# Kernel optimization log

Measured on AMD Instinct MI355X. Metric: run time of the kernel, lower is better.

Reference implementation:

```python
import jax, jax.numpy as jnp
import numpy as np

VOCAB, EMBED, HIDDEN, NCLASS = 50000, 256, 256, 5
B, T = 64, 512


def _lstm_cell(x, h, c, W, U, b):
    # Keras LSTMCell: gate order i, f, g(candidate), o
    z = x @ W + h @ U + b  # [B, 4H]
    i, f, g, o = jnp.split(z, 4, axis=-1)
    i = jax.nn.sigmoid(i)
    f = jax.nn.sigmoid(f)
    g = jnp.tanh(g)
    o = jax.nn.sigmoid(o)
    c_new = f * c + i * g
    h_new = o * jnp.tanh(c_new)
    return h_new, c_new


def _run_stacked(xs, W1, U1, b1, W2, U2, b2):
    # xs: [T, B, E] -> outputs of layer 2: [T, B, H]
    Bb = xs.shape[1]
    H = U1.shape[0]
    zero = jnp.zeros((Bb, H), dtype=xs.dtype)
    init = (zero, zero, zero, zero)

    def step(carry, x_t):
        h1, c1, h2, c2 = carry
        h1, c1 = _lstm_cell(x_t, h1, c1, W1, U1, b1)
        h2, c2 = _lstm_cell(h1, h2, c2, W2, U2, b2)
        return (h1, c1, h2, c2), h2

    _, ys = jax.lax.scan(step, init, xs)
    return ys


def setup_inputs() -> dict:
    key = jax.random.key(0)
    ks = jax.random.split(key, 16)
    s = 0.05

    def mk(k, shape):
        return (jax.random.normal(k, shape, dtype=jnp.float32) * s)

    inp = {
        "tokens": jax.random.randint(ks[0], (B, T), 0, VOCAB, dtype=jnp.int64),
        "embed_table": mk(ks[1], (VOCAB, EMBED)),
        # forward direction, layer 1 and 2
        "fw_W1": mk(ks[2], (EMBED, 4 * HIDDEN)),
        "fw_U1": mk(ks[3], (HIDDEN, 4 * HIDDEN)),
        "fw_b1": jnp.zeros((4 * HIDDEN,), jnp.float32),
        "fw_W2": mk(ks[4], (HIDDEN, 4 * HIDDEN)),
        "fw_U2": mk(ks[5], (HIDDEN, 4 * HIDDEN)),
        "fw_b2": jnp.zeros((4 * HIDDEN,), jnp.float32),
        # backward direction, layer 1 and 2
        "bw_W1": mk(ks[6], (EMBED, 4 * HIDDEN)),
        "bw_U1": mk(ks[7], (HIDDEN, 4 * HIDDEN)),
        "bw_b1": jnp.zeros((4 * HIDDEN,), jnp.float32),
        "bw_W2": mk(ks[8], (HIDDEN, 4 * HIDDEN)),
        "bw_U2": mk(ks[9], (HIDDEN, 4 * HIDDEN)),
        "bw_b2": jnp.zeros((4 * HIDDEN,), jnp.float32),
        # output dense (2H -> 5), softmax
        "dense_W": mk(ks[10], (2 * HIDDEN, NCLASS)),
        "dense_b": jnp.zeros((NCLASS,), jnp.float32),
    }
    return inp


def reference(tokens, embed_table,
              fw_W1, fw_U1, fw_b1, fw_W2, fw_U2, fw_b2,
              bw_W1, bw_U1, bw_b1, bw_W2, bw_U2, bw_b2,
              dense_W, dense_b):
    emb = embed_table[tokens]                    # [B, T, E]
    xs = jnp.swapaxes(emb, 0, 1)                 # [T, B, E]

    ys_fw = _run_stacked(xs, fw_W1, fw_U1, fw_b1, fw_W2, fw_U2, fw_b2)          # [T,B,H]
    ys_bw = _run_stacked(xs[::-1], bw_W1, bw_U1, bw_b1, bw_W2, bw_U2, bw_b2)[::-1]

    feat = jnp.concatenate([ys_fw, ys_bw], axis=-1)   # [T, B, 2H]
    feat = jnp.swapaxes(feat, 0, 1)                   # [B, T, 2H]
    logits = feat @ dense_W + dense_b                 # [B, T, 5]
    return jax.nn.softmax(logits, axis=-1)
```

## Files before the change

### kernel.cpp

```cpp
#include <hip/hip_runtime.h>

typedef __bf16 bf16;
typedef __bf16 bf16x8 __attribute__((ext_vector_type(8)));
typedef float f32x4 __attribute__((ext_vector_type(4)));
typedef unsigned long long u64;

#define T_LEN 512
#define BATCH 64
#define HID 256
#define LDA 520
#define ZLD 68

#define CTRL_BYTES 4096
#define LOG_OFF CTRL_BYTES
#define LOG_BYTES (T_LEN * BATCH * 16 * 5 * 4)
#define RING_OFF (LOG_OFF + LOG_BYTES)
#define HSLOT_U64 4096
#define RING_SLOTS 16
#define RING_U64 (RING_SLOTS * HSLOT_U64)
#define RING_BYTES (4 * RING_U64 * 8)

#define SMEM_A 66560
#define SMEM_Z 17408
#define SMEM_C 4096
#define SMEM_TAIL 576
#define SMEM_BYTES (SMEM_A + SMEM_Z + SMEM_C + SMEM_TAIL)

__device__ inline uint4 cvt8(const float4* s) {
    float4 a = s[0], b = s[1];
    union { uint4 u; bf16 h[8]; } r;
    r.h[0] = (bf16)a.x; r.h[1] = (bf16)a.y; r.h[2] = (bf16)a.z; r.h[3] = (bf16)a.w;
    r.h[4] = (bf16)b.x; r.h[5] = (bf16)b.y; r.h[6] = (bf16)b.z; r.h[7] = (bf16)b.w;
    return r.u;
}

__device__ __forceinline__ void load16(const u64* src, int tid, u64* dst) {
#pragma unroll
    for (int k = 0; k < 16; ++k)
        dst[k] = __hip_atomic_load(src + k * 256 + tid, __ATOMIC_RELAXED, __HIP_MEMORY_SCOPE_AGENT);
}

__device__ __forceinline__ void resolve16(const u64* src, int tid, unsigned ep,
                                          unsigned mask, u64* dst) {
    for (;;) {
        bool ok = true;
#pragma unroll
        for (int k = 0; k < 16; ++k)
            if ((mask >> k) & 1u) ok &= ((((unsigned)dst[k]) & 1u) == ep);
        if (__all(ok)) break;
        load16(src, tid, dst);
    }
}

__global__ void __launch_bounds__(256, 1)
lstm_kernel(const int* __restrict__ tokens,
            const float* __restrict__ embed,
            const float* __restrict__ W1f, const float* __restrict__ U1f, const float* __restrict__ b1f,
            const float* __restrict__ W2f, const float* __restrict__ U2f, const float* __restrict__ b2f,
            const float* __restrict__ W1b, const float* __restrict__ U1b, const float* __restrict__ b1b,
            const float* __restrict__ W2b, const float* __restrict__ U2b, const float* __restrict__ b2b,
            const float* __restrict__ dW,
            char* __restrict__ ws)
{
    extern __shared__ char smem[];
    bf16*  Abuf  = (bf16*)smem;
    float* zLds  = (float*)(smem + SMEM_A);
    float* cLds  = (float*)(smem + SMEM_A + SMEM_Z);
    float* bLds  = (float*)(smem + SMEM_A + SMEM_Z + SMEM_C);
    float* dwLds = bLds + 64;

    const int tid = threadIdx.x;
    const int wg  = blockIdx.x;
    const int dir = wg & 1, layer = (wg >> 1) & 1, sub = wg >> 2;

    const float *Wp, *Up, *bp;
    if (dir == 0) { if (layer == 0) { Wp=W1f; Up=U1f; bp=b1f; } else { Wp=W2f; Up=U2f; bp=b2f; } }
    else          { if (layer == 0) { Wp=W1b; Up=U1b; bp=b1b; } else { Wp=W2b; Up=U2b; bp=b2b; } }

    {
        for (int it = 0; it < 32; ++it) {
            int idx = it * 256 + tid;
            int k = idx >> 4, q4 = idx & 15;
            int g = q4 >> 2, u0 = (q4 & 3) * 4;
            const float* src = (k < 256) ? (Wp + (size_t)k * 1024 + g * 256 + sub * 16 + u0)
                                         : (Up + (size_t)(k - 256) * 1024 + g * 256 + sub * 16 + u0);
            float4 v = *(const float4*)src;
            int c0 = g * 16 + u0;
            Abuf[(c0 + 0) * LDA + k] = (bf16)v.x;
            Abuf[(c0 + 1) * LDA + k] = (bf16)v.y;
            Abuf[(c0 + 2) * LDA + k] = (bf16)v.z;
            Abuf[(c0 + 3) * LDA + k] = (bf16)v.w;
        }
        if (tid < 64) {
            int g = tid >> 4, u = tid & 15;
            bLds[tid] = bp[g * 256 + sub * 16 + u];
        }
        if (tid < 80) {
            int u = tid / 5, c = tid % 5;
            dwLds[tid] = dW[(size_t)(dir * 256 + sub * 16 + u) * 5 + c];
        }
        for (int i = tid; i < 1024; i += 256) cLds[i] = 0.f;
    }
    __syncthreads();

    const int wave = tid >> 6, lane = tid & 63, quad = lane >> 4, ln = lane & 15;
    const int mrow0 = (wave >> 1) * 32, ncol0 = (wave & 1) * 32;
    bf16x8 bfrag[2][16];
#pragma unroll
    for (int nt = 0; nt < 2; ++nt)
#pragma unroll
        for (int kt = 0; kt < 16; ++kt)
            bfrag[nt][kt] = *(const bf16x8*)&Abuf[(ncol0 + nt * 16 + ln) * LDA + kt * 32 + quad * 8];
    __syncthreads();

    u64* ringL1  = (u64*)(ws + RING_OFF) + (size_t)(dir * 2 + 0) * RING_U64;
    u64* ringL2  = (u64*)(ws + RING_OFF) + (size_t)(dir * 2 + 1) * RING_U64;
    u64* ringOwn = (layer == 0) ? ringL1 : ringL2;
    float* logits  = (float*)(ws + LOG_OFF);
    unsigned* prog = (unsigned*)ws + dir * 32;

    const int bA = tid >> 2, qA = tid & 3;
    const unsigned ownMask = 0xFFFFu ^ (1u << sub);
    unsigned progCache = 0u;
    u64 pkPrevW = 0ull;

    float4 pf[16];
    int tokB = 0;
    if (layer == 0) {
        const int tt0 = dir ? (T_LEN - 1) : 0;
        int tokA = tokens[bA * T_LEN + tt0];
        const float4* src = (const float4*)(embed + (size_t)tokA * HID + qA * 64);
#pragma unroll
        for (int j = 0; j < 16; ++j) pf[j] = src[j];
        const int tt1 = dir ? (T_LEN - 2) : 1;
        tokB = tokens[bA * T_LEN + tt1];
    }

    for (int s = 0; s < T_LEN; ++s) {
        u64 hreg[16], xreg[16];
        const u64* ownSrc = ringOwn + (size_t)(s & 15) * HSLOT_U64;
        const u64* xSrc   = ringL1 + (size_t)((s + 1) & 15) * HSLOT_U64;
        if (s > 0) load16(ownSrc, tid, hreg);
        if (layer == 1) load16(xSrc, tid, xreg);

        if (layer == 0 && tid == 0 && s >= 13) {
            unsigned need = (unsigned)(s - 12);
            while (progCache < need)
                progCache = __hip_atomic_load(prog, __ATOMIC_RELAXED, __HIP_MEMORY_SCOPE_AGENT);
        }

        if (s > 0) {
            resolve16(ownSrc, tid, (unsigned)(((s - 1) >> 4) & 1), ownMask, hreg);
        } else {
#pragma unroll
            for (int k = 0; k < 16; ++k) hreg[k] = 0ull;
        }
        hreg[sub] = pkPrevW;

        if (layer == 0) {
            uint4* dstx = (uint4*)&Abuf[bA * LDA + qA * 64];
#pragma unroll
            for (int j = 0; j < 8; ++j) dstx[j] = cvt8(&pf[2 * j]);
        } else {
            resolve16(xSrc, tid, (unsigned)((s >> 4) & 1), 0xFFFFu, xreg);
#pragma unroll
            for (int k = 0; k < 16; ++k)
                *(u64*)&Abuf[bA * LDA + k * 16 + qA * 4] = xreg[k];
        }
#pragma unroll
        for (int k = 0; k < 16; ++k)
            *(u64*)&Abuf[bA * LDA + 256 + k * 16 + qA * 4] = hreg[k];
        __syncthreads();

        if (layer == 0) {
            const float4* src = (const float4*)(embed + (size_t)tokB * HID + qA * 64);
#pragma unroll
            for (int j = 0; j < 16; ++j) pf[j] = src[j];
            const int sn2 = (s + 2 < T_LEN) ? s + 2 : T_LEN - 1;
            const int tt2 = dir ? (T_LEN - 1 - sn2) : sn2;
            tokB = tokens[bA * T_LEN + tt2];
        }

        f32x4 acc[2][2];
#pragma unroll
        for (int mi = 0; mi < 2; ++mi)
#pragma unroll
            for (int ni = 0; ni < 2; ++ni) acc[mi][ni] = (f32x4)(0.0f);
#pragma unroll
        for (int kt = 0; kt < 16; ++kt) {
            bf16x8 a0 = *(const bf16x8*)&Abuf[(mrow0 + ln) * LDA + kt * 32 + quad * 8];
            bf16x8 a1 = *(const bf16x8*)&Abuf[(mrow0 + 16 + ln) * LDA + kt * 32 + quad * 8];
            acc[0][0] = __builtin_amdgcn_mfma_f32_16x16x32_bf16(a0, bfrag[0][kt], acc[0][0], 0, 0, 0);
            acc[0][1] = __builtin_amdgcn_mfma_f32_16x16x32_bf16(a0, bfrag[1][kt], acc[0][1], 0, 0, 0);
            acc[1][0] = __builtin_amdgcn_mfma_f32_16x16x32_bf16(a1, bfrag[0][kt], acc[1][0], 0, 0, 0);
            acc[1][1] = __builtin_amdgcn_mfma_f32_16x16x32_bf16(a1, bfrag[1][kt], acc[1][1], 0, 0, 0);
        }
#pragma unroll
        for (int mi = 0; mi < 2; ++mi)
#pragma unroll
            for (int ni = 0; ni < 2; ++ni) {
                int row = mrow0 + mi * 16 + quad * 4;
                int col = ncol0 + ni * 16 + ln;
#pragma unroll
                for (int r = 0; r < 4; ++r)
                    zLds[(row + r) * ZLD + col] = acc[mi][ni][r];
            }
        __syncthreads();

        u64* hdst = ringOwn + (size_t)((s + 1) & 15) * HSLOT_U64;
        float hv[4];
        {
            const int b = bA, u0 = qA * 4;
#pragma unroll
            for (int e = 0; e < 4; ++e) {
                int u = u0 + e;
                float zi = zLds[b * ZLD + u]      + bLds[u];
                float zf = zLds[b * ZLD + 16 + u] + bLds[16 + u];
                float zg = zLds[b * ZLD + 32 + u] + bLds[32 + u];
                float zo = zLds[b * ZLD + 48 + u] + bLds[48 + u];
                float ig = 1.f / (1.f + __expf(-zi));
                float fg = 1.f / (1.f + __expf(-zf));
                float gg = 1.f - 2.f / (__expf(2.f * zg) + 1.f);
                float og = 1.f / (1.f + __expf(-zo));
                float cn = fg * cLds[b * 16 + u] + ig * gg;
                cLds[b * 16 + u] = cn;
                hv[e] = og * (1.f - 2.f / (__expf(2.f * cn) + 1.f));
            }
            union { u64 w; bf16 h[4]; } pk;
#pragma unroll
            for (int e = 0; e < 4; ++e) pk.h[e] = (bf16)hv[e];
            pk.w = (pk.w & ~1ull) | (u64)((s >> 4) & 1);
            pkPrevW = pk.w;
            __hip_atomic_store(hdst + sub * 256 + tid, pk.w,
                               __ATOMIC_RELAXED, __HIP_MEMORY_SCOPE_AGENT);
        }
        float pr[5];
        if (layer == 1) {
#pragma unroll
            for (int c = 0; c < 5; ++c)
                pr[c] = hv[0] * dwLds[(qA * 4 + 0) * 5 + c] + hv[1] * dwLds[(qA * 4 + 1) * 5 + c]
                      + hv[2] * dwLds[(qA * 4 + 2) * 5 + c] + hv[3] * dwLds[(qA * 4 + 3) * 5 + c];
#pragma unroll
            for (int m = 1; m < 4; m <<= 1)
#pragma unroll
                for (int c = 0; c < 5; ++c) pr[c] += __shfl_xor(pr[c], m);
        }

        if (layer == 1 && tid == 0)
            __hip_atomic_store(prog, (unsigned)(s + 1),
                               __ATOMIC_RELAXED, __HIP_MEMORY_SCOPE_AGENT);

        if (layer == 1 && qA == 0) {
            const int tp = dir ? (T_LEN - 1 - s) : s;
            float* lp = &logits[(((size_t)tp * BATCH + bA) * 16 + sub) * 5];
#pragma unroll
            for (int c = 0; c < 5; ++c) lp[c] = pr[c];
        }
    }
}

__global__ void __launch_bounds__(256)
softmax_kernel(const char* __restrict__ ws, const float* __restrict__ dB, float* __restrict__ out)
{
    const int gid = blockIdx.x * 256 + threadIdx.x;
    const int b = gid & 63, t = gid >> 6;
    const float* lp = (const float*)(ws + LOG_OFF) + ((size_t)t * BATCH + b) * 80;
    float l[5];
#pragma unroll
    for (int c = 0; c < 5; ++c) l[c] = dB[c];
#pragma unroll
    for (int sub = 0; sub < 16; ++sub)
#pragma unroll
        for (int c = 0; c < 5; ++c) l[c] += lp[sub * 5 + c];
    float m = l[0];
#pragma unroll
    for (int c = 1; c < 5; ++c) m = fmaxf(m, l[c]);
    float e[5], ssum = 0.f;
#pragma unroll
    for (int c = 0; c < 5; ++c) { e[c] = __expf(l[c] - m); ssum += e[c]; }
    float inv = 1.f / ssum;
    float* o = out + ((size_t)b * T_LEN + t) * 5;
#pragma unroll
    for (int c = 0; c < 5; ++c) o[c] = e[c] * inv;
}

extern "C" void kernel_launch(void* const* d_in, const int* in_sizes, int n_in,
                              void* d_out, int out_size, void* d_ws, size_t ws_size,
                              hipStream_t stream)
{
    const int*   tokens = (const int*)d_in[0];
    const float* embed  = (const float*)d_in[1];
    const float* W1f = (const float*)d_in[2],  *U1f = (const float*)d_in[3],  *b1f = (const float*)d_in[4];
    const float* W2f = (const float*)d_in[5],  *U2f = (const float*)d_in[6],  *b2f = (const float*)d_in[7];
    const float* W1b = (const float*)d_in[8],  *U1b = (const float*)d_in[9],  *b1b = (const float*)d_in[10];
    const float* W2b = (const float*)d_in[11], *U2b = (const float*)d_in[12], *b2b = (const float*)d_in[13];
    const float* dW  = (const float*)d_in[14], *dB  = (const float*)d_in[15];

    hipFuncSetAttribute(reinterpret_cast<const void*>(lstm_kernel),
                        hipFuncAttributeMaxDynamicSharedMemorySize, SMEM_BYTES);
    hipMemsetAsync(d_ws, 0, CTRL_BYTES, stream);
    hipMemsetAsync((char*)d_ws + RING_OFF, 0xFF, RING_BYTES, stream);
    lstm_kernel<<<dim3(64), dim3(256), SMEM_BYTES, stream>>>(
        tokens, embed, W1f, U1f, b1f, W2f, U2f, b2f,
        W1b, U1b, b1b, W2b, U2b, b2b, dW, (char*)d_ws);
    softmax_kernel<<<dim3(128), dim3(256), 0, stream>>>((const char*)d_ws, dB, (float*)d_out);
}
```

Measured before the change: 2.825 ms.

## Pin each LSTM direction to one XCD and exchange hidden state via L2-local ring

Launches 256 workgroups, reads the hardware XCC id, and assigns the 32 workgroups of each direction to a single XCD (with a fallback so any direction short of workgroups is filled from the rest). Surplus workgroups exit early. Hidden states are written with sc0 stores into the ring and also mirrored through agent-scope atomics, and polling alternates between the two with s_sleep backoff. The aim is to keep the per-step cross-workgroup exchange inside one XCD's L2 instead of going through device-coherent memory. This adds a startup barrier across all 256 workgroups, double stores per step, and relies on XCD scheduling behaviour. ZLD also changes from 68 to 67.

```diff
diff --git a/kernel.cpp b/kernel.cpp
--- a/kernel.cpp
+++ b/kernel.cpp
@@ -9,7 +9,9 @@
 #define BATCH 64
 #define HID 256
 #define LDA 520
-#define ZLD 68
+#define ZLD 67
+
+#define NTOTAL_WG 256
 
 #define CTRL_BYTES 4096
 #define LOG_OFF CTRL_BYTES
@@ -19,12 +21,15 @@
 #define RING_SLOTS 16
 #define RING_U64 (RING_SLOTS * HSLOT_U64)
 #define RING_BYTES (4 * RING_U64 * 8)
+#define MIR_OFF (RING_OFF + RING_BYTES)
 
 #define SMEM_A 66560
 #define SMEM_Z 17408
 #define SMEM_C 4096
 #define SMEM_TAIL 576
 #define SMEM_BYTES (SMEM_A + SMEM_Z + SMEM_C + SMEM_TAIL)
+
+#define HWREG_XCC_ID (((32 - 1) << 11) | (0 << 6) | 20)
 
 __device__ inline uint4 cvt8(const float4* s) {
     float4 a = s[0], b = s[1];
@@ -34,21 +39,50 @@
     return r.u;
 }
 
-__device__ __forceinline__ void load16(const u64* src, int tid, u64* dst) {
-#pragma unroll
-    for (int k = 0; k < 16; ++k)
-        dst[k] = __hip_atomic_load(src + k * 256 + tid, __ATOMIC_RELAXED, __HIP_MEMORY_SCOPE_AGENT);
-}
-
-__device__ __forceinline__ void resolve16(const u64* src, int tid, unsigned ep,
-                                          unsigned mask, u64* dst) {
+__device__ __forceinline__ void issue16(const u64* src, int tid, u64 (&d)[16]) {
+#pragma unroll
+    for (int k = 0; k < 16; ++k) {
+        const u64* p = src + (size_t)k * 256 + tid;
+        asm volatile("global_load_dwordx2 %0, %1, off sc0"
+                     : "=&v"(d[k]) : "v"((u64)p));
+    }
+}
+
+__device__ __forceinline__ void waitvm0() {
+    asm volatile("s_waitcnt vmcnt(0)" ::: "memory");
+    __builtin_amdgcn_sched_barrier(0);
+}
+
+__device__ __forceinline__ void store_sc0(u64* p, u64 v) {
+    asm volatile("global_store_dwordx2 %0, %1, off sc0" :: "v"((u64)p), "v"(v) : "memory");
+}
+
+__device__ __forceinline__ void resolve_dual(const u64* ring, const u64* mir, int tid,
+                                             unsigned ep, unsigned mask, u64 (&d)[16]) {
+    int pass = 0;
     for (;;) {
         bool ok = true;
 #pragma unroll
         for (int k = 0; k < 16; ++k)
-            if ((mask >> k) & 1u) ok &= ((((unsigned)dst[k]) & 1u) == ep);
+            if ((mask >> k) & 1u) ok &= ((((unsigned)d[k]) & 1u) == ep);
         if (__all(ok)) break;
-        load16(src, tid, dst);
+        __builtin_amdgcn_s_sleep(1);
+        if (pass & 1) {
+#pragma unroll
+            for (int k = 0; k < 16; ++k) {
+                u64 v = __hip_atomic_load(mir + (size_t)k * 256 + tid,
+                                          __ATOMIC_RELAXED, __HIP_MEMORY_SCOPE_AGENT);
+                if ((((unsigned)d[k]) & 1u) != ep) d[k] = v;
+            }
+        } else {
+            u64 t[16];
+            issue16(ring, tid, t);
+            waitvm0();
+#pragma unroll
+            for (int k = 0; k < 16; ++k)
+                if ((((unsigned)d[k]) & 1u) != ep) d[k] = t[k];
+        }
+        ++pass;
     }
 }
 
@@ -70,8 +104,41 @@
     float* dwLds = bLds + 64;
 
     const int tid = threadIdx.x;
-    const int wg  = blockIdx.x;
-    const int dir = wg & 1, layer = (wg >> 1) & 1, sub = wg >> 2;
+
+    int* roleSh = (int*)zLds;
+    if (tid == 0) {
+        unsigned* cnt = (unsigned*)ws + 256;
+        int xcd = __builtin_amdgcn_s_getreg(HWREG_XCC_ID) & 15;
+        int dir = -1, slot = -1;
+        unsigned pj = 0xFFFFFFFFu;
+        if (xcd == 0 || xcd == 1) {
+            unsigned sl = __hip_atomic_fetch_add(cnt + xcd, 1u,
+                              __ATOMIC_RELAXED, __HIP_MEMORY_SCOPE_AGENT);
+            if (sl < 32u) { dir = xcd; slot = (int)sl; }
+        }
+        if (dir < 0)
+            pj = __hip_atomic_fetch_add(cnt + 2, 1u,
+                     __ATOMIC_RELAXED, __HIP_MEMORY_SCOPE_AGENT);
+        __hip_atomic_fetch_add(cnt + 3, 1u, __ATOMIC_RELEASE, __HIP_MEMORY_SCOPE_AGENT);
+        while (__hip_atomic_load(cnt + 3, __ATOMIC_ACQUIRE, __HIP_MEMORY_SCOPE_AGENT) < 256u)
+            __builtin_amdgcn_s_sleep(1);
+        if (dir < 0) {
+            unsigned nA = __hip_atomic_load(cnt + 0, __ATOMIC_RELAXED, __HIP_MEMORY_SCOPE_AGENT);
+            unsigned nB = __hip_atomic_load(cnt + 1, __ATOMIC_RELAXED, __HIP_MEMORY_SCOPE_AGENT);
+            nA = nA < 32u ? nA : 32u; nB = nB < 32u ? nB : 32u;
+            unsigned missA = 32u - nA, missB = 32u - nB;
+            if (pj < missA)              { dir = 0; slot = (int)(nA + pj); }
+            else if (pj < missA + missB) { dir = 1; slot = (int)(nB + (pj - missA)); }
+        }
+        roleSh[0] = dir;
+        roleSh[1] = slot;
+    }
+    __syncthreads();
+    const int dir  = roleSh[0];
+    const int slot = roleSh[1];
+    __syncthreads();
+    if (dir < 0) return;
+    const int layer = slot & 1, sub = slot >> 1;
 
     const float *Wp, *Up, *bp;
     if (dir == 0) { if (layer == 0) { Wp=W1f; Up=U1f; bp=b1f; } else { Wp=W2f; Up=U2f; bp=b2f; } }
@@ -113,9 +180,10 @@
             bfrag[nt][kt] = *(const bf16x8*)&Abuf[(ncol0 + nt * 16 + ln) * LDA + kt * 32 + quad * 8];
     __syncthreads();
 
-    u64* ringL1  = (u64*)(ws + RING_OFF) + (size_t)(dir * 2 + 0) * RING_U64;
-    u64* ringL2  = (u64*)(ws + RING_OFF) + (size_t)(dir * 2 + 1) * RING_U64;
-    u64* ringOwn = (layer == 0) ? ringL1 : ringL2;
+    u64* ringL1 = (u64*)(ws + RING_OFF) + (size_t)(dir * 2 + 0) * RING_U64;
+    u64* mirL1  = (u64*)(ws + MIR_OFF)  + (size_t)(dir * 2 + 0) * RING_U64;
+    u64* ringOwn = (u64*)(ws + RING_OFF) + (size_t)(dir * 2 + layer) * RING_U64;
+    u64* mirOwn  = (u64*)(ws + MIR_OFF)  + (size_t)(dir * 2 + layer) * RING_U64;
     float* logits  = (float*)(ws + LOG_OFF);
     unsigned* prog = (unsigned*)ws + dir * 32;
 
@@ -138,10 +206,13 @@
 
     for (int s = 0; s < T_LEN; ++s) {
         u64 hreg[16], xreg[16];
-        const u64* ownSrc = ringOwn + (size_t)(s & 15) * HSLOT_U64;
-        const u64* xSrc   = ringL1 + (size_t)((s + 1) & 15) * HSLOT_U64;
-        if (s > 0) load16(ownSrc, tid, hreg);
-        if (layer == 1) load16(xSrc, tid, xreg);
+        const u64* ownRing = ringOwn + (size_t)(s & 15) * HSLOT_U64;
+        const u64* ownMir  = mirOwn  + (size_t)(s & 15) * HSLOT_U64;
+        const u64* xRing   = ringL1 + (size_t)((s + 1) & 15) * HSLOT_U64;
+        const u64* xMir    = mirL1  + (size_t)((s + 1) & 15) * HSLOT_U64;
+        if (s > 0) issue16(ownRing, tid, hreg);
+        if (layer == 1) issue16(xRing, tid, xreg);
+        if (s > 0 || layer == 1) waitvm0();
 
         if (layer == 0 && tid == 0 && s >= 13) {
             unsigned need = (unsigned)(s - 12);
@@ -150,7 +221,7 @@
         }
 
         if (s > 0) {
-            resolve16(ownSrc, tid, (unsigned)(((s - 1) >> 4) & 1), ownMask, hreg);
+            resolve_dual(ownRing, ownMir, tid, (unsigned)(((s - 1) >> 4) & 1), ownMask, hreg);
         } else {
 #pragma unroll
             for (int k = 0; k < 16; ++k) hreg[k] = 0ull;
@@ -162,7 +233,7 @@
 #pragma unroll
             for (int j = 0; j < 8; ++j) dstx[j] = cvt8(&pf[2 * j]);
         } else {
-            resolve16(xSrc, tid, (unsigned)((s >> 4) & 1), 0xFFFFu, xreg);
+            resolve_dual(xRing, xMir, tid, (unsigned)((s >> 4) & 1), 0xFFFFu, xreg);
 #pragma unroll
             for (int k = 0; k < 16; ++k)
                 *(u64*)&Abuf[bA * LDA + k * 16 + qA * 4] = xreg[k];
@@ -207,7 +278,7 @@
             }
         __syncthreads();
 
-        u64* hdst = ringOwn + (size_t)((s + 1) & 15) * HSLOT_U64;
+        const size_t dstOff = (size_t)((s + 1) & 15) * HSLOT_U64 + (size_t)sub * 256 + tid;
         float hv[4];
         {
             const int b = bA, u0 = qA * 4;
@@ -231,7 +302,8 @@
             for (int e = 0; e < 4; ++e) pk.h[e] = (bf16)hv[e];
             pk.w = (pk.w & ~1ull) | (u64)((s >> 4) & 1);
             pkPrevW = pk.w;
-            __hip_atomic_store(hdst + sub * 256 + tid, pk.w,
+            store_sc0(ringOwn + dstOff, pk.w);
+            __hip_atomic_store(mirOwn + dstOff, pk.w,
                                __ATOMIC_RELAXED, __HIP_MEMORY_SCOPE_AGENT);
         }
         float pr[5];
@@ -299,8 +371,8 @@
     hipFuncSetAttribute(reinterpret_cast<const void*>(lstm_kernel),
                         hipFuncAttributeMaxDynamicSharedMemorySize, SMEM_BYTES);
     hipMemsetAsync(d_ws, 0, CTRL_BYTES, stream);
-    hipMemsetAsync((char*)d_ws + RING_OFF, 0xFF, RING_BYTES, stream);
-    lstm_kernel<<<dim3(64), dim3(256), SMEM_BYTES, stream>>>(
+    hipMemsetAsync((char*)d_ws + RING_OFF, 0xFF, 2 * RING_BYTES, stream);
+    lstm_kernel<<<dim3(NTOTAL_WG), dim3(256), SMEM_BYTES, stream>>>(
         tokens, embed, W1f, U1f, b1f, W2f, U2f, b2f,
         W1b, U1b, b1b, W2b, U2b, b2b, dW, (char*)d_ws);
     softmax_kernel<<<dim3(128), dim3(256), 0, stream>>>((const char*)d_ws, dB, (float*)d_out);
```

Measured after the change: 3.174 ms. 12.4% more time.
